# Optimization experiments

Measured on AMD Instinct MI355X. Metric: run time of the kernel, lower is better.

The kernel has to match this reference:

```python
import jax, jax.numpy as jnp
import numpy as np

CUTOFF = 0.05

def _freq_filter(x_chw, filter_type):
    # x_chw: [C,H,W] = batch element 0, detached in the original (stop_gradient)
    x = jax.lax.stop_gradient(x_chw)
    C, H, W = x.shape
    a = jnp.abs(x)
    mn = a.min(axis=(1, 2), keepdims=True)
    ptp = a.max(axis=(1, 2), keepdims=True) - mn
    # np.uint8(255*(a-mn)/ptp): values in [0,255], cast truncates -> floor
    q = jnp.floor(255.0 * (a - mn) / ptp)
    f = jnp.fft.fftshift(jnp.fft.fft2(q), axes=(-2, -1))
    crow, ccol = H // 2, W // 2
    dr, dc = int(CUTOFF * crow), int(CUTOFF * ccol)
    m = jnp.zeros((H, W), dtype=q.dtype)
    m = m.at[crow - dr:crow + dr, ccol - dc:ccol + dc].set(1.0)
    if filter_type == 'low_pass':
        m = 1.0 - m  # note: original 'low_pass' actually removes low freqs
    out = jnp.abs(jnp.fft.ifft2(jnp.fft.ifftshift(f * m, axes=(-2, -1))))
    return out.astype(x_chw.dtype)  # [C,H,W]

def _conv1x1(x, w, b):
    # x: [B,C,H,W], w: [O,C], b: [O]
    return jnp.einsum('oc,bchw->bohw', w, x) + b[None, :, None, None]

def setup_inputs() -> dict:
    key = jax.random.key(0)
    ks = jax.random.split(key, 7)
    B, C, H, W = 1, 256, 96, 96
    fuse = jax.random.normal(ks[0], (B, C, H, W), dtype=jnp.float32)
    s = 1.0 / np.sqrt(C)
    Wq = jax.random.normal(ks[1], (C, C), dtype=jnp.float32) * s
    bq = jax.random.normal(ks[2], (C,), dtype=jnp.float32) * 0.01
    Wk = jax.random.normal(ks[3], (C, C), dtype=jnp.float32) * s
    bk = jax.random.normal(ks[4], (C,), dtype=jnp.float32) * 0.01
    Wv = jax.random.normal(ks[5], (C, C), dtype=jnp.float32) * s
    bv = jax.random.normal(ks[6], (C,), dtype=jnp.float32) * 0.01
    return {"fuse": fuse, "Wq": Wq, "bq": bq, "Wk": Wk, "bk": bk, "Wv": Wv, "bv": bv}

def reference(fuse, Wq, bq, Wk, bk, Wv, bv):
    B, C, H, W = fuse.shape
    scale = 1.0 / (C ** 0.5)
    # frequency-filtered maps (computed from batch 0, broadcast to all batches)
    FQ = jnp.broadcast_to(_freq_filter(fuse[0], 'high_pass'), fuse.shape)
    FK = jnp.broadcast_to(_freq_filter(fuse[0], 'low_pass'), fuse.shape)
    fuse_Query = _conv1x1(FQ, Wq, bq).reshape(B, C, H * W)     # [B,C,HW]
    fuse_Q_mask = fuse_Query.reshape(B * H, C * W)             # [B*H, C*W]
    fuse_Query_t = jnp.transpose(fuse_Query, (0, 2, 1))        # [B,HW,C]
    fuse_Key = _conv1x1(FK, Wk, bk).reshape(B, C, H * W)       # [B,C,HW]
    Fuse_Q_mask = jnp.max(fuse_Q_mask, axis=0, keepdims=True)  # [1, C*W]
    mask_KQ = jnp.einsum('bnc,bcm->bnm', fuse_Query_t, fuse_Key) * scale  # [B,HW,HW]
    mask_KQ = jax.nn.softmax(mask_KQ, axis=0)  # softmax over batch dim (as in original)
    mask_KQ = jnp.max(mask_KQ, axis=1)                         # [B,HW]
    mask_KQ = mask_KQ.reshape(-1, W)                           # [B*H, W]
    mask_KQ = jnp.max(mask_KQ, axis=-1, keepdims=True)         # [B*H, 1]
    mask = (mask_KQ @ Fuse_Q_mask).reshape(B, C, H, W)
    fuse_Value = _conv1x1(fuse, Wv, bv)
    return fuse_Value + fuse_Value * mask
```

## Files before the change

kernel.cpp:

```cpp
#include <hip/hip_runtime.h>
#include <math.h>

#define CCH 256
#define HW  9216
#define CW  24576
#define TWO_PI 6.28318530717958647692f

typedef __attribute__((ext_vector_type(8))) short short8;
typedef __attribute__((ext_vector_type(4))) float f32x4;

__device__ inline unsigned short f2bf(float f) {
    unsigned u = __float_as_uint(f);
    unsigned r = (u + 0x7FFFu + ((u >> 16) & 1u)) >> 16;
    return (unsigned short)r;
}

__global__ __launch_bounds__(768) void k_pre(const float* __restrict__ x,
                                             const float* __restrict__ Wq,
                                             const float* __restrict__ Wv,
                                             short8* __restrict__ Wqt,
                                             short8* __restrict__ Wvt,
                                             unsigned* __restrict__ FQm,
                                             float* __restrict__ Fg) {
    __shared__ float qa[HW];
    __shared__ float cs[96][2];
    __shared__ float Gp[8][96][5];
    __shared__ float Gs[96][6];
    __shared__ float red[24];
    __shared__ float s_mn, s_ptp;
    int bid = blockIdx.x, t = threadIdx.x;

    if (bid >= 256) {
        int widx = bid - 256;
        if (t < 256) {
            const float* src = (widx >= 32) ? Wv : Wq;
            short8* dst = (widx >= 32) ? Wvt : Wqt;
            int cidx = (widx & 31) * 256 + t;
            int ot = cidx >> 11, kc = (cidx >> 6) & 31, m = cidx & 63;
            const float* s = src + (ot * 64 + m) * 256 + kc * 8;
            short8 v;
            #pragma unroll
            for (int e = 0; e < 8; ++e) v[e] = (short)f2bf(s[e]);
            dst[cidx] = v;
        }
        return;
    }

    int c = bid;
    if (t < 96) FQm[c * 96 + t] = 0u;
    const float* xp = x + c * HW;
    if (t < 96) { float a = TWO_PI * (float)t / 96.0f; cs[t][0] = cosf(a); cs[t][1] = sinf(a); }
    float lo = 1e30f, hi = 0.f;
    #pragma unroll
    for (int i = 0; i < 12; ++i) {
        float a = fabsf(xp[t + i * 768]);
        qa[t + i * 768] = a;
        lo = fminf(lo, a);
        hi = fmaxf(hi, a);
    }
    #pragma unroll
    for (int d = 32; d; d >>= 1) {
        lo = fminf(lo, __shfl_xor(lo, d, 64));
        hi = fmaxf(hi, __shfl_xor(hi, d, 64));
    }
    if ((t & 63) == 0) { red[t >> 6] = lo; red[12 + (t >> 6)] = hi; }
    __syncthreads();
    if (t == 0) {
        lo = red[0]; hi = red[12];
        #pragma unroll
        for (int i = 1; i < 12; ++i) { lo = fminf(lo, red[i]); hi = fmaxf(hi, red[12 + i]); }
        s_mn = lo; s_ptp = hi - lo;
    }
    __syncthreads();
    float mn = s_mn, ptp = s_ptp;

    {
        int xx = t % 96, h = t / 96;
        float g0r = 0, g0i = 0, g1r = 0, g1i = 0, g2 = 0;
        for (int y = h * 12; y < h * 12 + 12; ++y) {
            float q = floorf(255.0f * (qa[y * 96 + xx] - mn) / ptp);
            float c1 = cs[y][0], s1 = cs[y][1];
            float c2 = c1 * c1 - s1 * s1, s2 = 2.0f * c1 * s1;
            g0r += q * c2; g0i += q * s2;
            g1r += q * c1; g1i += q * s1;
            g2  += q;
        }
        Gp[h][xx][0] = g0r; Gp[h][xx][1] = g0i;
        Gp[h][xx][2] = g1r; Gp[h][xx][3] = g1i;
        Gp[h][xx][4] = g2;
    }
    __syncthreads();
    if (t < 96) {
        #pragma unroll
        for (int j = 0; j < 5; ++j) {
            float s = 0.f;
            #pragma unroll
            for (int h = 0; h < 8; ++h) s += Gp[h][t][j];
            Gs[t][j] = s;
        }
        Gs[t][5] = 0.f;
    }
    __syncthreads();
    if (t < 64) {
        int coef = t >> 2, qq = t & 3;
        int ky = coef >> 2, kx = coef & 3;
        float fr = 0, fi = 0;
        for (int xx = qq * 24; xx < qq * 24 + 24; ++xx) {
            float c1 = cs[xx][0], s1 = cs[xx][1];
            float er, ei;
            if (kx == 0)      { er = c1 * c1 - s1 * s1; ei = 2.0f * c1 * s1; }
            else if (kx == 1) { er = c1; ei = s1; }
            else if (kx == 2) { er = 1.f; ei = 0.f; }
            else              { er = c1; ei = -s1; }
            float gr, gi;
            if (ky == 0)      { gr = Gs[xx][0]; gi = Gs[xx][1]; }
            else if (ky == 1) { gr = Gs[xx][2]; gi = Gs[xx][3]; }
            else if (ky == 2) { gr = Gs[xx][4]; gi = 0.f; }
            else              { gr = Gs[xx][2]; gi = -Gs[xx][3]; }
            fr += gr * er - gi * ei;
            fi += gr * ei + gi * er;
        }
        fr += __shfl_xor(fr, 1, 64); fr += __shfl_xor(fr, 2, 64);
        fi += __shfl_xor(fi, 1, 64); fi += __shfl_xor(fi, 2, 64);
        if (qq == 0) {
            Fg[c * 32 + 2 * coef]     = fr;
            Fg[c * 32 + 2 * coef + 1] = fi;
        }
    }
}

__global__ __launch_bounds__(256) void k_gemmQV(const short8* __restrict__ Wqt,
                                                const short8* __restrict__ Wvt,
                                                const float* __restrict__ Fg,
                                                const float* __restrict__ bq,
                                                const float* __restrict__ bv,
                                                const float* __restrict__ x,
                                                unsigned* __restrict__ FQm,
                                                float* __restrict__ out) {
    __shared__ short8 As[2048];
    __shared__ short8 Bs[2048];
    __shared__ float Rs[2048][2];
    float (*fq)[64] = (float (*)[64])Rs;
    int tid = threadIdx.x;
    int pt_ = blockIdx.x;
    bool isQ = blockIdx.y < 4;
    int ot = isQ ? blockIdx.y : blockIdx.y - 4;
    const short8* wsrc = (isQ ? Wqt : Wvt) + ot * 2048;
    #pragma unroll
    for (int i = 0; i < 8; ++i) As[i * 256 + tid] = wsrc[i * 256 + tid];

    int p0 = pt_ * 64;
    if (isQ) {
        int y0 = p0 / 96;
        {
            int yi = (tid >> 2) & 1, kx = tid & 3, cb = tid >> 3;
            float ay = TWO_PI * (float)(y0 + yi) / 96.0f;
            float cyv = cosf(ay), syv = sinf(ay);
            float cy2 = cyv * cyv - syv * syv, sy2 = 2.f * cyv * syv;
            float Ur[4] = { cy2, cyv, 1.f, cyv };
            float Ui[4] = { -sy2, -syv, 0.f, syv };
            #pragma unroll
            for (int i = 0; i < 8; ++i) {
                int cc = cb + i * 32;
                float rr = 0.f, ri = 0.f;
                #pragma unroll
                for (int ky = 0; ky < 4; ++ky) {
                    float fr = Fg[cc * 32 + 2 * (ky * 4 + kx)];
                    float fi = Fg[cc * 32 + 2 * (ky * 4 + kx) + 1];
                    rr += fr * Ur[ky] - fi * Ui[ky];
                    ri += fr * Ui[ky] + fi * Ur[ky];
                }
                Rs[cc * 8 + yi * 4 + kx][0] = rr;
                Rs[cc * 8 + yi * 4 + kx][1] = ri;
            }
        }
        __syncthreads();
        const float inv = 1.0f / 9216.0f;
        #pragma unroll
        for (int i = 0; i < 8; ++i) {
            int si = i * 256 + tid;
            int kcg = si >> 6, n = si & 63;
            int p = p0 + n;
            int y = p / 96, xx = p - y * 96;
            int yi = y - y0;
            float axv = TWO_PI * (float)xx / 96.0f;
            float cxv = cosf(axv), sxv = sinf(axv);
            float cx2 = cxv * cxv - sxv * sxv, sx2 = 2.f * cxv * sxv;
            float Tr[4] = { cx2, cxv, 1.f, cxv };
            float Ti[4] = { -sx2, -sxv, 0.f, sxv };
            short8 vv;
            #pragma unroll
            for (int e = 0; e < 8; ++e) {
                int rb = (kcg * 8 + e) * 8 + yi * 4;
                float ar = 0.f, ai = 0.f;
                #pragma unroll
                for (int kx = 0; kx < 4; ++kx) {
                    float rr = Rs[rb + kx][0], ri = Rs[rb + kx][1];
                    ar += rr * Tr[kx] - ri * Ti[kx];
                    ai += rr * Ti[kx] + ri * Tr[kx];
                }
                vv[e] = (short)f2bf(sqrtf(ar * ar + ai * ai) * inv);
            }
            Bs[si] = vv;
        }
    } else {
        #pragma unroll
        for (int i = 0; i < 8; ++i) {
            int si = i * 256 + tid;
            int KC = si >> 6, n = si & 63;
            const float* xb = x + (size_t)(KC * 8) * HW + p0 + n;
            short8 v;
            #pragma unroll
            for (int e = 0; e < 8; ++e) v[e] = (short)f2bf(xb[(size_t)e * HW]);
            Bs[si] = v;
        }
    }
    __syncthreads();

    int l = tid & 63, w = tid >> 6;
    int wr = w >> 1, wc = w & 1;
    int l15 = l & 15, quad = l >> 4;
    f32x4 acc[2][2] = {};
    int abase = wr * 32 + l15;
    int bbase = wc * 32 + l15;
    #pragma unroll
    for (int s = 0; s < 8; ++s) {
        int kc = s * 4 + quad;
        short8 a0 = As[kc * 64 + abase];
        short8 a1 = As[kc * 64 + abase + 16];
        short8 b0 = Bs[kc * 64 + bbase];
        short8 b1 = Bs[kc * 64 + bbase + 16];
        acc[0][0] = __builtin_amdgcn_mfma_f32_16x16x32_bf16(a0, b0, acc[0][0], 0, 0, 0);
        acc[0][1] = __builtin_amdgcn_mfma_f32_16x16x32_bf16(a0, b1, acc[0][1], 0, 0, 0);
        acc[1][0] = __builtin_amdgcn_mfma_f32_16x16x32_bf16(a1, b0, acc[1][0], 0, 0, 0);
        acc[1][1] = __builtin_amdgcn_mfma_f32_16x16x32_bf16(a1, b1, acc[1][1], 0, 0, 0);
    }

    if (isQ) {
        float vloc[2][4];
        #pragma unroll
        for (int ni = 0; ni < 2; ++ni) {
            #pragma unroll
            for (int r = 0; r < 4; ++r) {
                int o_lo = ot * 64 + wr * 32 + quad * 4 + r;
                float v = fmaxf(acc[0][ni][r] + bq[o_lo], acc[1][ni][r] + bq[o_lo + 16]);
                v = fmaxf(v, __shfl_xor(v, 32, 64));
                vloc[ni][r] = v;
            }
        }
        if (wr == 0 && quad < 2) {
            #pragma unroll
            for (int ni = 0; ni < 2; ++ni)
                #pragma unroll
                for (int r = 0; r < 4; ++r)
                    fq[quad * 4 + r][wc * 32 + ni * 16 + l15] = vloc[ni][r];
        }
        __syncthreads();
        if (wr == 1 && quad < 2) {
            #pragma unroll
            for (int ni = 0; ni < 2; ++ni) {
                #pragma unroll
                for (int r = 0; r < 4; ++r) {
                    int row = quad * 4 + r;
                    int col = wc * 32 + ni * 16 + l15;
                    float v = fmaxf(vloc[ni][r], fq[row][col]);
                    int p = pt_ * 64 + col;
                    int k = row * HW + p;
                    if (k >= CW) k -= CW;
                    if (k >= CW) k -= CW;
                    unsigned u = __float_as_uint(v);
                    unsigned key = (u & 0x80000000u) ? ~u : (u | 0x80000000u);
                    atomicMax(&FQm[k], key);
                }
            }
        }
    } else {
        #pragma unroll
        for (int mi = 0; mi < 2; ++mi) {
            #pragma unroll
            for (int ni = 0; ni < 2; ++ni) {
                #pragma unroll
                for (int r = 0; r < 4; ++r) {
                    int o = ot * 64 + wr * 32 + mi * 16 + quad * 4 + r;
                    int p = pt_ * 64 + wc * 32 + ni * 16 + l15;
                    out[(size_t)o * HW + p] = acc[mi][ni][r] + bv[o];
                }
            }
        }
    }
}

__device__ inline float mdecode(unsigned key) {
    unsigned ub = (key & 0x80000000u) ? (key ^ 0x80000000u) : ~key;
    return __uint_as_float(ub);
}
__global__ __launch_bounds__(256) void k_mask(float* __restrict__ out,
                                              const unsigned* __restrict__ FQm) {
    int i = (blockIdx.x * 256 + threadIdx.x) * 8;
    int o = i / HW;
    int p = i - o * HW;
    int k = (o & 7) * HW + p;
    if (k >= CW) k -= CW;
    if (k >= CW) k -= CW;
    float4 v0 = *(const float4*)(out + i);
    float4 v1 = *(const float4*)(out + i + 4);
    uint4 k0 = *(const uint4*)(FQm + k);
    uint4 k1 = *(const uint4*)(FQm + k + 4);
    v0.x *= 1.0f + mdecode(k0.x); v0.y *= 1.0f + mdecode(k0.y);
    v0.z *= 1.0f + mdecode(k0.z); v0.w *= 1.0f + mdecode(k0.w);
    v1.x *= 1.0f + mdecode(k1.x); v1.y *= 1.0f + mdecode(k1.y);
    v1.z *= 1.0f + mdecode(k1.z); v1.w *= 1.0f + mdecode(k1.w);
    *(float4*)(out + i)     = v0;
    *(float4*)(out + i + 4) = v1;
}

extern "C" void kernel_launch(void* const* d_in, const int* in_sizes, int n_in,
                              void* d_out, int out_size, void* d_ws, size_t ws_size,
                              hipStream_t stream) {
    const float* fuse = (const float*)d_in[0];
    const float* Wq   = (const float*)d_in[1];
    const float* bq   = (const float*)d_in[2];
    const float* Wv   = (const float*)d_in[5];
    const float* bv   = (const float*)d_in[6];
    float* out = (float*)d_out;

    char* ws = (char*)d_ws;
    unsigned* FQm = (unsigned*)(ws);
    float*    Fg  = (float*)(ws + 98304);
    short8*   Wqt = (short8*)(ws + 131072);
    short8*   Wvt = (short8*)(ws + 262144);

    k_pre<<<320, 768, 0, stream>>>(fuse, Wq, Wv, Wqt, Wvt, FQm, Fg);
    k_gemmQV<<<dim3(144, 8), 256, 0, stream>>>(Wqt, Wvt, Fg, bq, bv, fuse, FQm, out);
    k_mask<<<1152, 256, 0, stream>>>(out, FQm);
}
```

Measured before the change: 115.1 us.

## Compute Q filtered tile once per block and loop over all output tiles

Q blocks now build the frequency-filtered B tile once and loop over all four output-channel tiles, instead of four separate blocks each recomputing the costly inverse-DFT reconstruction. Weight tiles for the next output tile are prefetched into registers while the current one is used, and the running max is kept in registers, so atomics drop from four blocks per pixel tile to one. The grid shrinks from 8 to 5 rows in y. The trade-off is that Q blocks now run serially longer, with fewer blocks available for parallelism and possible load imbalance against the V blocks.

```diff
diff --git a/kernel.cpp b/kernel.cpp
--- a/kernel.cpp
+++ b/kernel.cpp
@@ -143,14 +143,20 @@
     float (*fq)[64] = (float (*)[64])Rs;
     int tid = threadIdx.x;
     int pt_ = blockIdx.x;
-    bool isQ = blockIdx.y < 4;
-    int ot = isQ ? blockIdx.y : blockIdx.y - 4;
-    const short8* wsrc = (isQ ? Wqt : Wvt) + ot * 2048;
-    #pragma unroll
-    for (int i = 0; i < 8; ++i) As[i * 256 + tid] = wsrc[i * 256 + tid];
-
+    bool isQ = blockIdx.y == 0;
     int p0 = pt_ * 64;
+
+    int l = tid & 63, w = tid >> 6;
+    int wr = w >> 1, wc = w & 1;
+    int l15 = l & 15, quad = l >> 4;
+    int abase = wr * 32 + l15;
+    int bbase = wc * 32 + l15;
+
     if (isQ) {
+        short8 areg[8];
+        #pragma unroll
+        for (int i = 0; i < 8; ++i) areg[i] = Wqt[i * 256 + tid];
+
         int y0 = p0 / 96;
         {
             int yi = (tid >> 2) & 1, kx = tid & 3, cb = tid >> 3;
@@ -203,26 +209,100 @@
             }
             Bs[si] = vv;
         }
-    } else {
-        #pragma unroll
-        for (int i = 0; i < 8; ++i) {
-            int si = i * 256 + tid;
-            int KC = si >> 6, n = si & 63;
-            const float* xb = x + (size_t)(KC * 8) * HW + p0 + n;
-            short8 v;
-            #pragma unroll
-            for (int e = 0; e < 8; ++e) v[e] = (short)f2bf(xb[(size_t)e * HW]);
-            Bs[si] = v;
-        }
-    }
-    __syncthreads();
-
-    int l = tid & 63, w = tid >> 6;
-    int wr = w >> 1, wc = w & 1;
-    int l15 = l & 15, quad = l >> 4;
+        __syncthreads();
+
+        float vmax[2][4];
+        #pragma unroll
+        for (int ni = 0; ni < 2; ++ni)
+            #pragma unroll
+            for (int r = 0; r < 4; ++r) vmax[ni][r] = -3.0e38f;
+
+        #pragma unroll
+        for (int ot = 0; ot < 4; ++ot) {
+            #pragma unroll
+            for (int i = 0; i < 8; ++i) As[i * 256 + tid] = areg[i];
+            __syncthreads();
+            if (ot < 3) {
+                #pragma unroll
+                for (int i = 0; i < 8; ++i) areg[i] = Wqt[(ot + 1) * 2048 + i * 256 + tid];
+            }
+            f32x4 acc[2][2] = {};
+            #pragma unroll
+            for (int s = 0; s < 8; ++s) {
+                int kc = s * 4 + quad;
+                short8 a0 = As[kc * 64 + abase];
+                short8 a1 = As[kc * 64 + abase + 16];
+                short8 b0 = Bs[kc * 64 + bbase];
+                short8 b1 = Bs[kc * 64 + bbase + 16];
+                acc[0][0] = __builtin_amdgcn_mfma_f32_16x16x32_bf16(a0, b0, acc[0][0], 0, 0, 0);
+                acc[0][1] = __builtin_amdgcn_mfma_f32_16x16x32_bf16(a0, b1, acc[0][1], 0, 0, 0);
+                acc[1][0] = __builtin_amdgcn_mfma_f32_16x16x32_bf16(a1, b0, acc[1][0], 0, 0, 0);
+                acc[1][1] = __builtin_amdgcn_mfma_f32_16x16x32_bf16(a1, b1, acc[1][1], 0, 0, 0);
+            }
+            #pragma unroll
+            for (int ni = 0; ni < 2; ++ni) {
+                #pragma unroll
+                for (int r = 0; r < 4; ++r) {
+                    int o_lo = ot * 64 + wr * 32 + quad * 4 + r;
+                    float v = fmaxf(acc[0][ni][r] + bq[o_lo], acc[1][ni][r] + bq[o_lo + 16]);
+                    vmax[ni][r] = fmaxf(vmax[ni][r], v);
+                }
+            }
+            __syncthreads();
+        }
+
+        #pragma unroll
+        for (int ni = 0; ni < 2; ++ni)
+            #pragma unroll
+            for (int r = 0; r < 4; ++r)
+                vmax[ni][r] = fmaxf(vmax[ni][r], __shfl_xor(vmax[ni][r], 32, 64));
+        if (wr == 0 && quad < 2) {
+            #pragma unroll
+            for (int ni = 0; ni < 2; ++ni)
+                #pragma unroll
+                for (int r = 0; r < 4; ++r)
+                    fq[quad * 4 + r][wc * 32 + ni * 16 + l15] = vmax[ni][r];
+        }
+        __syncthreads();
+        if (wr == 1 && quad < 2) {
+            #pragma unroll
+            for (int ni = 0; ni < 2; ++ni) {
+                #pragma unroll
+                for (int r = 0; r < 4; ++r) {
+                    int row = quad * 4 + r;
+                    int col = wc * 32 + ni * 16 + l15;
+                    float v = fmaxf(vmax[ni][r], fq[row][col]);
+                    int p = p0 + col;
+                    int k = row * HW + p;
+                    if (k >= CW) k -= CW;
+                    if (k >= CW) k -= CW;
+                    unsigned u = __float_as_uint(v);
+                    unsigned key = (u & 0x80000000u) ? ~u : (u | 0x80000000u);
+                    atomicMax(&FQm[k], key);
+                }
+            }
+        }
+        return;
+    }
+
+    int ot = blockIdx.y - 1;
+    const short8* wsrc = Wvt + ot * 2048;
+    #pragma unroll
+    for (int i = 0; i < 8; ++i) As[i * 256 + tid] = wsrc[i * 256 + tid];
+
+    #pragma unroll
+    for (int i = 0; i < 8; ++i) {
+        int si = i * 256 + tid;
+        int KC = si >> 6, n = si & 63;
+        const float* xb = x + (size_t)(KC * 8) * HW + p0 + n;
+        short8 v;
+        #pragma unroll
+        for (int e = 0; e < 8; ++e) v[e] = (short)f2bf(xb[(size_t)e * HW]);
+        Bs[si] = v;
+    }
+    __syncthreads();
+
     f32x4 acc[2][2] = {};
-    int abase = wr * 32 + l15;
-    int bbase = wc * 32 + l15;
     #pragma unroll
     for (int s = 0; s < 8; ++s) {
         int kc = s * 4 + quad;
@@ -236,55 +316,15 @@
         acc[1][1] = __builtin_amdgcn_mfma_f32_16x16x32_bf16(a1, b1, acc[1][1], 0, 0, 0);
     }
 
-    if (isQ) {
-        float vloc[2][4];
+    #pragma unroll
+    for (int mi = 0; mi < 2; ++mi) {
         #pragma unroll
         for (int ni = 0; ni < 2; ++ni) {
             #pragma unroll
             for (int r = 0; r < 4; ++r) {
-                int o_lo = ot * 64 + wr * 32 + quad * 4 + r;
-                float v = fmaxf(acc[0][ni][r] + bq[o_lo], acc[1][ni][r] + bq[o_lo + 16]);
-                v = fmaxf(v, __shfl_xor(v, 32, 64));
-                vloc[ni][r] = v;
-            }
-        }
-        if (wr == 0 && quad < 2) {
-            #pragma unroll
-            for (int ni = 0; ni < 2; ++ni)
-                #pragma unroll
-                for (int r = 0; r < 4; ++r)
-                    fq[quad * 4 + r][wc * 32 + ni * 16 + l15] = vloc[ni][r];
-        }
-        __syncthreads();
-        if (wr == 1 && quad < 2) {
-            #pragma unroll
-            for (int ni = 0; ni < 2; ++ni) {
-                #pragma unroll
-                for (int r = 0; r < 4; ++r) {
-                    int row = quad * 4 + r;
-                    int col = wc * 32 + ni * 16 + l15;
-                    float v = fmaxf(vloc[ni][r], fq[row][col]);
-                    int p = pt_ * 64 + col;
-                    int k = row * HW + p;
-                    if (k >= CW) k -= CW;
-                    if (k >= CW) k -= CW;
-                    unsigned u = __float_as_uint(v);
-                    unsigned key = (u & 0x80000000u) ? ~u : (u | 0x80000000u);
-                    atomicMax(&FQm[k], key);
-                }
-            }
-        }
-    } else {
-        #pragma unroll
-        for (int mi = 0; mi < 2; ++mi) {
-            #pragma unroll
-            for (int ni = 0; ni < 2; ++ni) {
-                #pragma unroll
-                for (int r = 0; r < 4; ++r) {
-                    int o = ot * 64 + wr * 32 + mi * 16 + quad * 4 + r;
-                    int p = pt_ * 64 + wc * 32 + ni * 16 + l15;
-                    out[(size_t)o * HW + p] = acc[mi][ni][r] + bv[o];
-                }
+                int o = ot * 64 + wr * 32 + mi * 16 + quad * 4 + r;
+                int p = p0 + wc * 32 + ni * 16 + l15;
+                out[(size_t)o * HW + p] = acc[mi][ni][r] + bv[o];
             }
         }
     }
@@ -331,6 +371,6 @@
     short8*   Wvt = (short8*)(ws + 262144);
 
     k_pre<<<320, 768, 0, stream>>>(fuse, Wq, Wv, Wqt, Wvt, FQm, Fg);
-    k_gemmQV<<<dim3(144, 8), 256, 0, stream>>>(Wqt, Wvt, Fg, bq, bv, fuse, FQm, out);
+    k_gemmQV<<<dim3(144, 5), 256, 0, stream>>>(Wqt, Wvt, Fg, bq, bv, fuse, FQm, out);
     k_mask<<<1152, 256, 0, stream>>>(out, FQm);
 }
```

Result: faster. 103.5 us (-10.1%).
